# Performance work log

Measured on AMD Instinct MI355X. Metric: run time of the kernel, lower is better.

Reference implementation:

```python
import jax, jax.numpy as jnp
import numpy as np
from jax import lax

INPUT_SIZE = 32
HIDDEN = 64
BATCH = 8192
SEQ = 128


def _lstm_layer(x, w_ih, w_hh, b_ih, b_hh):
    """Single unidirectional LSTM layer, PyTorch gate order (i, f, g, o).
    x: [B, T, D] -> (outputs [B, T, H], final h [B, H])"""
    B = x.shape[0]
    H = w_hh.shape[1]
    # Precompute input contributions for all timesteps: [B, T, 4H]
    xg = jnp.einsum('btd,gd->btg', x, w_ih) + b_ih + b_hh

    def step(carry, xg_t):
        h, c = carry
        gates = xg_t + h @ w_hh.T  # [B, 4H]
        i, f, g, o = jnp.split(gates, 4, axis=-1)
        i = jax.nn.sigmoid(i)
        f = jax.nn.sigmoid(f)
        g = jnp.tanh(g)
        o = jax.nn.sigmoid(o)
        c = f * c + i * g
        h = o * jnp.tanh(c)
        return (h, c), h

    h0 = jnp.zeros((B, H), dtype=x.dtype)
    c0 = jnp.zeros((B, H), dtype=x.dtype)
    (h_n, _), hs = lax.scan(step, (h0, c0), jnp.swapaxes(xg, 0, 1))
    return jnp.swapaxes(hs, 0, 1), h_n


def setup_inputs() -> dict:
    key = jax.random.key(0)
    ks = jax.random.split(key, 12)
    H4 = 4 * HIDDEN
    s_ih0 = 1.0 / np.sqrt(INPUT_SIZE)
    s_h = 1.0 / np.sqrt(HIDDEN)
    x = jax.random.normal(ks[0], (BATCH, SEQ, INPUT_SIZE), dtype=jnp.float32)
    # Biases: zeros with forget-gate bias = 1 (per _init_weights)
    b = jnp.zeros((H4,), dtype=jnp.float32).at[HIDDEN:2 * HIDDEN].set(1.0)
    return {
        'x': x,
        'w_ih0': jax.random.uniform(ks[1], (H4, INPUT_SIZE), jnp.float32, -s_ih0, s_ih0),
        'w_hh0': jax.random.uniform(ks[2], (H4, HIDDEN), jnp.float32, -s_h, s_h),
        'b_ih0': b,
        'b_hh0': jnp.zeros((H4,), dtype=jnp.float32),
        'w_ih1': jax.random.uniform(ks[3], (H4, HIDDEN), jnp.float32, -s_h, s_h),
        'w_hh1': jax.random.uniform(ks[4], (H4, HIDDEN), jnp.float32, -s_h, s_h),
        'b_ih1': b,
        'b_hh1': jnp.zeros((H4,), dtype=jnp.float32),
        'fc_w': jax.random.uniform(ks[5], (1, HIDDEN), jnp.float32, -s_h, s_h),
        'fc_b': jnp.zeros((1,), dtype=jnp.float32),
    }


def reference(x, w_ih0, w_hh0, b_ih0, b_hh0, w_ih1, w_hh1, b_ih1, b_hh1, fc_w, fc_b):
    # 2-layer LSTM (inter-layer dropout is identity at inference)
    h1_seq, _ = _lstm_layer(x, w_ih0, w_hh0, b_ih0, b_hh0)
    _, h_final = _lstm_layer(h1_seq, w_ih1, w_hh1, b_ih1, b_hh1)
    # dropout(h_final) is identity in eval mode; final linear head -> squeeze
    logit = h_final @ fc_w.T + fc_b  # [B, 1]
    return logit.squeeze(-1)  # [B]
```

## Files before the change

### kernel.cpp

```cpp
#include <hip/hip_runtime.h>


#define TT  128
#define DIN 32
#define BT  16
#define L2E 1.44269504088896340736f

typedef _Float16 h8 __attribute__((ext_vector_type(8)));
typedef __fp16   p2 __attribute__((ext_vector_type(2)));
typedef float    f4 __attribute__((ext_vector_type(4)));

__device__ __forceinline__ h8 cvt8s(const float* p, float s) {
    float4 a = *(const float4*)p;
    float4 b = *(const float4*)(p + 4);
    union { h8 v; p2 q[4]; } u;
    u.q[0] = __builtin_amdgcn_cvt_pkrtz(a.x * s, a.y * s);
    u.q[1] = __builtin_amdgcn_cvt_pkrtz(a.z * s, a.w * s);
    u.q[2] = __builtin_amdgcn_cvt_pkrtz(b.x * s, b.y * s);
    u.q[3] = __builtin_amdgcn_cvt_pkrtz(b.z * s, b.w * s);
    return u.v;
}

__device__ __forceinline__ h8 pack8(const float4& a, const float4& b) {
    union { h8 v; p2 q[4]; } u;
    u.q[0] = __builtin_amdgcn_cvt_pkrtz(a.x, a.y);
    u.q[1] = __builtin_amdgcn_cvt_pkrtz(a.z, a.w);
    u.q[2] = __builtin_amdgcn_cvt_pkrtz(b.x, b.y);
    u.q[3] = __builtin_amdgcn_cvt_pkrtz(b.z, b.w);
    return u.v;
}

__device__ __forceinline__ float elem(const f4& acc, float& c) {
    float Ei = __builtin_amdgcn_exp2f(-acc[0]);
    float Ef = __builtin_amdgcn_exp2f(-acc[1]);
    float Eg = __builtin_amdgcn_exp2f(-acc[2]);
    float Eo = __builtin_amdgcn_exp2f(-acc[3]);
    float a = 1.f + Ei, b = 1.f + Eg, d = 1.f + Ef;
    float P = a * b;
    float N = c * P + (1.f - Eg) * d;
    c = N * __builtin_amdgcn_rcpf(P * d);
    float Ec = __builtin_amdgcn_exp2f(-2.f * L2E * c);
    return (1.f - Ec) * __builtin_amdgcn_rcpf((1.f + Ec) * (1.f + Eo));
}

__global__ __launch_bounds__(512, 4)
void lstm2_fused(const float* __restrict__ x,
                 const float* __restrict__ wih0, const float* __restrict__ whh0,
                 const float* __restrict__ bih0, const float* __restrict__ bhh0,
                 const float* __restrict__ wih1, const float* __restrict__ whh1,
                 const float* __restrict__ bih1, const float* __restrict__ bhh1,
                 const float* __restrict__ fcw,  const float* __restrict__ fcb,
                 float* __restrict__ out)
{
    const int tid  = threadIdx.x;
    const int lane = tid & 63;
    const int wv   = tid >> 6;
    const int bl   = lane & 15;
    const int kg   = lane >> 4;

    __shared__ alignas(16) unsigned short hb[2][2][BT * 64];
    __shared__ float wpart[8][BT];

    for (int i = tid; i < (int)(sizeof(hb) / 4); i += 512) ((int*)hb)[i] = 0;

    h8 W0[2][3], W1[2][4];
    f4 b0v[2], b1v[2];
    #pragma unroll
    for (int t = 0; t < 2; ++t) {
        const int hbse = 8 * wv + 4 * t;
        const int gam  = bl & 3;
        const int g    = 64 * gam + hbse + (bl >> 2);
        const float sc = (gam == 2) ? 2.f * L2E : L2E;
        W0[t][0] = cvt8s(wih0 + g * 32 + 8 * kg, sc);
        W0[t][1] = cvt8s(whh0 + g * 64 + 8 * kg, sc);
        W0[t][2] = cvt8s(whh0 + g * 64 + 32 + 8 * kg, sc);
        W1[t][0] = cvt8s(wih1 + g * 64 + 8 * kg, sc);
        W1[t][1] = cvt8s(wih1 + g * 64 + 32 + 8 * kg, sc);
        W1[t][2] = cvt8s(whh1 + g * 64 + 8 * kg, sc);
        W1[t][3] = cvt8s(whh1 + g * 64 + 32 + 8 * kg, sc);
        #pragma unroll
        for (int r = 0; r < 4; ++r) {
            const int gr = 64 * r + hbse + kg;
            const float scr = (r == 2) ? 2.f * L2E : L2E;
            b0v[t][r] = (bih0[gr] + bhh0[gr]) * scr;
            b1v[t][r] = (bih1[gr] + bhh1[gr]) * scr;
        }
    }

    const int bbase = blockIdx.x * BT;
    const float* xp = x + (size_t)(bbase + bl) * (TT * DIN) + 8 * kg;

    float c0[2] = {0.f, 0.f}, c1[2] = {0.f, 0.f}, h1f[2] = {0.f, 0.f};

    __syncthreads();

    const int swz = (bl & 7) << 4;
    char* lb = (char*)hb;
    const int rowoff = bl * 128;
    const int rd0 = rowoff + ((16 * kg) ^ swz);
    const int rd1 = rowoff + ((64 + 16 * kg) ^ swz);
    const int wro0 = rowoff + ((16 * wv + 2 * kg) ^ swz);
    const int wro1 = rowoff + ((16 * wv + 8 + 2 * kg) ^ swz);

    auto L0 = [&](const h8& xc, const h8& hr0, const h8& hr1, int wp) {
        #pragma unroll
        for (int t = 0; t < 2; ++t) {
            f4 acc = b0v[t];
            acc = __builtin_amdgcn_mfma_f32_16x16x32_f16(W0[t][1], hr0, acc, 0, 0, 0);
            acc = __builtin_amdgcn_mfma_f32_16x16x32_f16(W0[t][2], hr1, acc, 0, 0, 0);
            acc = __builtin_amdgcn_mfma_f32_16x16x32_f16(W0[t][0], xc,  acc, 0, 0, 0);
            float h = elem(acc, c0[t]);
            *(_Float16*)(lb + wp * 2048 + (t ? wro1 : wro0)) = (_Float16)h;
        }
    };

    auto L1 = [&](const h8& g0a, const h8& g0b, const h8& g1a, const h8& g1b,
                  int wp, bool store) {
        #pragma unroll
        for (int t = 0; t < 2; ++t) {
            f4 acc = b1v[t];
            acc = __builtin_amdgcn_mfma_f32_16x16x32_f16(W1[t][0], g0a, acc, 0, 0, 0);
            acc = __builtin_amdgcn_mfma_f32_16x16x32_f16(W1[t][1], g0b, acc, 0, 0, 0);
            acc = __builtin_amdgcn_mfma_f32_16x16x32_f16(W1[t][2], g1a, acc, 0, 0, 0);
            acc = __builtin_amdgcn_mfma_f32_16x16x32_f16(W1[t][3], g1b, acc, 0, 0, 0);
            float h = elem(acc, c1[t]);
            h1f[t] = h;
            if (store) *(_Float16*)(lb + 4096 + wp * 2048 + (t ? wro1 : wro0)) = (_Float16)h;
        }
    };

    h8 xcur;
    {
        float4 x0a = *(const float4*)(xp);
        float4 x0b = *(const float4*)(xp + 4);
        float4 xnA = *(const float4*)(xp + DIN);
        float4 xnB = *(const float4*)(xp + DIN + 4);
        h8 xc  = pack8(x0a, x0b);
        h8 hr0 = *(const h8*)(lb + 2048 + rd0);
        h8 hr1 = *(const h8*)(lb + 2048 + rd1);
        L0(xc, hr0, hr1, 0);
        xcur = pack8(xnA, xnB);
        __syncthreads();
    }

    for (int it = 1; it < TT; ++it) {
        const int wp = it & 1, rp = wp ^ 1;
        const int tn = (it + 1 < TT) ? it + 1 : TT - 1;
        float4 xnA = *(const float4*)(xp + tn * DIN);
        float4 xnB = *(const float4*)(xp + tn * DIN + 4);

        h8 hr0 = *(const h8*)(lb + rp * 2048 + rd0);
        h8 hr1 = *(const h8*)(lb + rp * 2048 + rd1);
        h8 g1a = *(const h8*)(lb + 4096 + rp * 2048 + rd0);
        h8 g1b = *(const h8*)(lb + 4096 + rp * 2048 + rd1);

        L0(xcur, hr0, hr1, wp);
        L1(hr0, hr1, g1a, g1b, wp, true);

        xcur = pack8(xnA, xnB);
        __syncthreads();
    }

    {
        const int rp = 1;
        h8 hr0 = *(const h8*)(lb + rp * 2048 + rd0);
        h8 hr1 = *(const h8*)(lb + rp * 2048 + rd1);
        h8 g1a = *(const h8*)(lb + 4096 + rp * 2048 + rd0);
        h8 g1b = *(const h8*)(lb + 4096 + rp * 2048 + rd1);
        L1(hr0, hr1, g1a, g1b, 0, false);
    }

    float part = h1f[0] * fcw[8 * wv + kg] + h1f[1] * fcw[8 * wv + 4 + kg];
    part += __shfl_xor(part, 16, 64);
    part += __shfl_xor(part, 32, 64);
    if (lane < 16) wpart[wv][lane] = part;
    __syncthreads();
    if (tid < BT) {
        float s = fcb[0];
        #pragma unroll
        for (int w = 0; w < 8; ++w) s += wpart[w][tid];
        out[bbase + tid] = s;
    }
}

extern "C" void kernel_launch(void* const* d_in, const int* in_sizes, int n_in,
                              void* d_out, int out_size, void* d_ws, size_t ws_size,
                              hipStream_t stream) {
    (void)in_sizes; (void)n_in; (void)d_ws; (void)ws_size; (void)out_size;
    lstm2_fused<<<dim3(8192 / BT), dim3(512), 0, stream>>>(
        (const float*)d_in[0],
        (const float*)d_in[1], (const float*)d_in[2],
        (const float*)d_in[3], (const float*)d_in[4],
        (const float*)d_in[5], (const float*)d_in[6],
        (const float*)d_in[7], (const float*)d_in[8],
        (const float*)d_in[9], (const float*)d_in[10],
        (float*)d_out);
}
```

Before: 184.9 us.

## Split LSTM layers into producer/consumer warp groups with LDS flag sync

Assigns waves 0-3 to layer 0 and waves 4-7 to layer 1, each computing four hidden tiles, so the two layers run as a pipeline instead of in lockstep. Per-step __syncthreads is replaced by LDS counters polled with s_sleep, and layer-0 outputs go into a 4-deep ring buffer so the producer can run ahead. The aim is to overlap the two layers' dependency chains and cut block-wide barrier cost. In exchange it adds spin-wait polling, more registers per wave (weights for four tiles), and relies on volatile LDS ordering being correct.

```diff
diff --git a/kernel.cpp b/kernel.cpp
--- a/kernel.cpp
+++ b/kernel.cpp
@@ -9,6 +9,8 @@
 typedef _Float16 h8 __attribute__((ext_vector_type(8)));
 typedef __fp16   p2 __attribute__((ext_vector_type(2)));
 typedef float    f4 __attribute__((ext_vector_type(4)));
+
+#define MFMA(A, B, C) __builtin_amdgcn_mfma_f32_16x16x32_f16((A), (B), (C), 0, 0, 0)
 
 __device__ __forceinline__ h8 cvt8s(const float* p, float s) {
     float4 a = *(const float4*)p;
@@ -41,6 +43,17 @@
     c = N * __builtin_amdgcn_rcpf(P * d);
     float Ec = __builtin_amdgcn_exp2f(-2.f * L2E * c);
     return (1.f - Ec) * __builtin_amdgcn_rcpf((1.f + Ec) * (1.f + Eo));
+}
+
+__device__ __forceinline__ void waitmin4(const volatile int* c, int target) {
+    for (;;) {
+        int m0 = c[0], m1 = c[1], m2 = c[2], m3 = c[3];
+        int m = min(min(m0, m1), min(m2, m3));
+        if (m >= target) break;
+        __builtin_amdgcn_s_sleep(1);
+    }
+    __builtin_amdgcn_sched_barrier(0);
+    asm volatile("" ::: "memory");
 }
 
 __global__ __launch_bounds__(512, 4)
@@ -58,129 +71,157 @@
     const int bl   = lane & 15;
     const int kg   = lane >> 4;
 
-    __shared__ alignas(16) unsigned short hb[2][2][BT * 64];
-    __shared__ float wpart[8][BT];
+    __shared__ alignas(16) unsigned short hb[6][BT * 64];
+    __shared__ alignas(16) int ctrP[4];
+    __shared__ alignas(16) int ctrC[4];
+    __shared__ float wpart[4][BT];
 
     for (int i = tid; i < (int)(sizeof(hb) / 4); i += 512) ((int*)hb)[i] = 0;
-
-    h8 W0[2][3], W1[2][4];
-    f4 b0v[2], b1v[2];
-    #pragma unroll
-    for (int t = 0; t < 2; ++t) {
-        const int hbse = 8 * wv + 4 * t;
-        const int gam  = bl & 3;
-        const int g    = 64 * gam + hbse + (bl >> 2);
-        const float sc = (gam == 2) ? 2.f * L2E : L2E;
-        W0[t][0] = cvt8s(wih0 + g * 32 + 8 * kg, sc);
-        W0[t][1] = cvt8s(whh0 + g * 64 + 8 * kg, sc);
-        W0[t][2] = cvt8s(whh0 + g * 64 + 32 + 8 * kg, sc);
-        W1[t][0] = cvt8s(wih1 + g * 64 + 8 * kg, sc);
-        W1[t][1] = cvt8s(wih1 + g * 64 + 32 + 8 * kg, sc);
-        W1[t][2] = cvt8s(whh1 + g * 64 + 8 * kg, sc);
-        W1[t][3] = cvt8s(whh1 + g * 64 + 32 + 8 * kg, sc);
-        #pragma unroll
-        for (int r = 0; r < 4; ++r) {
-            const int gr = 64 * r + hbse + kg;
-            const float scr = (r == 2) ? 2.f * L2E : L2E;
-            b0v[t][r] = (bih0[gr] + bhh0[gr]) * scr;
-            b1v[t][r] = (bih1[gr] + bhh1[gr]) * scr;
-        }
-    }
+    if (tid < 4) { ctrP[tid] = 0; ctrC[tid] = 0; }
 
     const int bbase = blockIdx.x * BT;
-    const float* xp = x + (size_t)(bbase + bl) * (TT * DIN) + 8 * kg;
-
-    float c0[2] = {0.f, 0.f}, c1[2] = {0.f, 0.f}, h1f[2] = {0.f, 0.f};
-
-    __syncthreads();
-
     const int swz = (bl & 7) << 4;
     char* lb = (char*)hb;
     const int rowoff = bl * 128;
     const int rd0 = rowoff + ((16 * kg) ^ swz);
     const int rd1 = rowoff + ((64 + 16 * kg) ^ swz);
-    const int wro0 = rowoff + ((16 * wv + 2 * kg) ^ swz);
-    const int wro1 = rowoff + ((16 * wv + 8 + 2 * kg) ^ swz);
-
-    auto L0 = [&](const h8& xc, const h8& hr0, const h8& hr1, int wp) {
+
+    volatile int* vP = ctrP;
+    volatile int* vC = ctrC;
+
+    __syncthreads();
+
+    if (wv < 4) {
+        const int w = wv;
+        h8 W0[4][3]; f4 b0v[4]; int wro[4];
         #pragma unroll
-        for (int t = 0; t < 2; ++t) {
-            f4 acc = b0v[t];
-            acc = __builtin_amdgcn_mfma_f32_16x16x32_f16(W0[t][1], hr0, acc, 0, 0, 0);
-            acc = __builtin_amdgcn_mfma_f32_16x16x32_f16(W0[t][2], hr1, acc, 0, 0, 0);
-            acc = __builtin_amdgcn_mfma_f32_16x16x32_f16(W0[t][0], xc,  acc, 0, 0, 0);
-            float h = elem(acc, c0[t]);
-            *(_Float16*)(lb + wp * 2048 + (t ? wro1 : wro0)) = (_Float16)h;
-        }
-    };
-
-    auto L1 = [&](const h8& g0a, const h8& g0b, const h8& g1a, const h8& g1b,
-                  int wp, bool store) {
+        for (int t = 0; t < 4; ++t) {
+            const int hbse = 16 * w + 4 * t;
+            const int gam  = bl & 3;
+            const int g    = 64 * gam + hbse + (bl >> 2);
+            const float sc = (gam == 2) ? 2.f * L2E : L2E;
+            W0[t][0] = cvt8s(wih0 + g * 32 + 8 * kg, sc);
+            W0[t][1] = cvt8s(whh0 + g * 64 + 8 * kg, sc);
+            W0[t][2] = cvt8s(whh0 + g * 64 + 32 + 8 * kg, sc);
+            #pragma unroll
+            for (int r = 0; r < 4; ++r) {
+                const int gr = 64 * r + hbse + kg;
+                const float scr = (r == 2) ? 2.f * L2E : L2E;
+                b0v[t][r] = (bih0[gr] + bhh0[gr]) * scr;
+            }
+            wro[t] = rowoff + ((32 * w + 8 * t + 2 * kg) ^ swz);
+        }
+
+        const float* xp = x + (size_t)(bbase + bl) * (TT * DIN) + 8 * kg;
+        h8 xcur = pack8(*(const float4*)xp, *(const float4*)(xp + 4));
+        float c0[4] = {0.f, 0.f, 0.f, 0.f};
+
+        for (int t = 0; t < TT; ++t) {
+            if (t)      waitmin4(vP, t);
+            if (t >= 4) waitmin4(vC, t - 3);
+
+            const char* src = lb + (((t - 1) & 3) * 2048);
+            h8 hr0 = *(const h8*)(src + rd0);
+            h8 hr1 = *(const h8*)(src + rd1);
+            const int tn = (t + 1 < TT) ? t + 1 : t;
+            float4 xnA = *(const float4*)(xp + tn * DIN);
+            float4 xnB = *(const float4*)(xp + tn * DIN + 4);
+
+            __builtin_amdgcn_s_setprio(1);
+            f4 acc[4];
+            #pragma unroll
+            for (int k = 0; k < 4; ++k) {
+                acc[k] = b0v[k];
+                acc[k] = MFMA(W0[k][1], hr0, acc[k]);
+                acc[k] = MFMA(W0[k][2], hr1, acc[k]);
+                acc[k] = MFMA(W0[k][0], xcur, acc[k]);
+            }
+            __builtin_amdgcn_s_setprio(0);
+
+            char* dst = lb + ((t & 3) * 2048);
+            #pragma unroll
+            for (int k = 0; k < 4; ++k) {
+                float h = elem(acc[k], c0[k]);
+                *(_Float16*)(dst + wro[k]) = (_Float16)h;
+            }
+
+            asm volatile("s_waitcnt lgkmcnt(0)" ::: "memory");
+            if (lane == 0) vP[w] = t + 1;
+            xcur = pack8(xnA, xnB);
+        }
+    } else {
+        const int w = wv - 4;
+        h8 W1[4][4]; f4 b1v[4]; int wro[4];
         #pragma unroll
-        for (int t = 0; t < 2; ++t) {
-            f4 acc = b1v[t];
-            acc = __builtin_amdgcn_mfma_f32_16x16x32_f16(W1[t][0], g0a, acc, 0, 0, 0);
-            acc = __builtin_amdgcn_mfma_f32_16x16x32_f16(W1[t][1], g0b, acc, 0, 0, 0);
-            acc = __builtin_amdgcn_mfma_f32_16x16x32_f16(W1[t][2], g1a, acc, 0, 0, 0);
-            acc = __builtin_amdgcn_mfma_f32_16x16x32_f16(W1[t][3], g1b, acc, 0, 0, 0);
-            float h = elem(acc, c1[t]);
-            h1f[t] = h;
-            if (store) *(_Float16*)(lb + 4096 + wp * 2048 + (t ? wro1 : wro0)) = (_Float16)h;
-        }
-    };
-
-    h8 xcur;
-    {
-        float4 x0a = *(const float4*)(xp);
-        float4 x0b = *(const float4*)(xp + 4);
-        float4 xnA = *(const float4*)(xp + DIN);
-        float4 xnB = *(const float4*)(xp + DIN + 4);
-        h8 xc  = pack8(x0a, x0b);
-        h8 hr0 = *(const h8*)(lb + 2048 + rd0);
-        h8 hr1 = *(const h8*)(lb + 2048 + rd1);
-        L0(xc, hr0, hr1, 0);
-        xcur = pack8(xnA, xnB);
-        __syncthreads();
+        for (int t = 0; t < 4; ++t) {
+            const int hbse = 16 * w + 4 * t;
+            const int gam  = bl & 3;
+            const int g    = 64 * gam + hbse + (bl >> 2);
+            const float sc = (gam == 2) ? 2.f * L2E : L2E;
+            W1[t][0] = cvt8s(wih1 + g * 64 + 8 * kg, sc);
+            W1[t][1] = cvt8s(wih1 + g * 64 + 32 + 8 * kg, sc);
+            W1[t][2] = cvt8s(whh1 + g * 64 + 8 * kg, sc);
+            W1[t][3] = cvt8s(whh1 + g * 64 + 32 + 8 * kg, sc);
+            #pragma unroll
+            for (int r = 0; r < 4; ++r) {
+                const int gr = 64 * r + hbse + kg;
+                const float scr = (r == 2) ? 2.f * L2E : L2E;
+                b1v[t][r] = (bih1[gr] + bhh1[gr]) * scr;
+            }
+            wro[t] = rowoff + ((32 * w + 8 * t + 2 * kg) ^ swz);
+        }
+
+        float c1[4] = {0.f, 0.f, 0.f, 0.f};
+        float h1f[4] = {0.f, 0.f, 0.f, 0.f};
+
+        for (int t = 0; t < TT; ++t) {
+            waitmin4(vP, t + 1);
+            if (t) waitmin4(vC, t);
+
+            const char* s0 = lb + ((t & 3) * 2048);
+            const char* s1 = lb + 8192 + (((t - 1) & 1) * 2048);
+            h8 g0a = *(const h8*)(s0 + rd0);
+            h8 g0b = *(const h8*)(s0 + rd1);
+            h8 g1a = *(const h8*)(s1 + rd0);
+            h8 g1b = *(const h8*)(s1 + rd1);
+
+            __builtin_amdgcn_s_setprio(1);
+            f4 acc[4];
+            #pragma unroll
+            for (int k = 0; k < 4; ++k) {
+                acc[k] = b1v[k];
+                acc[k] = MFMA(W1[k][0], g0a, acc[k]);
+                acc[k] = MFMA(W1[k][1], g0b, acc[k]);
+                acc[k] = MFMA(W1[k][2], g1a, acc[k]);
+                acc[k] = MFMA(W1[k][3], g1b, acc[k]);
+            }
+            __builtin_amdgcn_s_setprio(0);
+
+            char* dst = lb + 8192 + ((t & 1) * 2048);
+            #pragma unroll
+            for (int k = 0; k < 4; ++k) {
+                float h = elem(acc[k], c1[k]);
+                h1f[k] = h;
+                if (t < TT - 1) *(_Float16*)(dst + wro[k]) = (_Float16)h;
+            }
+
+            if (t < TT - 1) {
+                asm volatile("s_waitcnt lgkmcnt(0)" ::: "memory");
+                if (lane == 0) vC[w] = t + 1;
+            }
+        }
+
+        float part = 0.f;
+        #pragma unroll
+        for (int k = 0; k < 4; ++k) part += h1f[k] * fcw[16 * w + 4 * k + kg];
+        part += __shfl_xor(part, 16, 64);
+        part += __shfl_xor(part, 32, 64);
+        if (lane < 16) wpart[w][lane] = part;
     }
 
-    for (int it = 1; it < TT; ++it) {
-        const int wp = it & 1, rp = wp ^ 1;
-        const int tn = (it + 1 < TT) ? it + 1 : TT - 1;
-        float4 xnA = *(const float4*)(xp + tn * DIN);
-        float4 xnB = *(const float4*)(xp + tn * DIN + 4);
-
-        h8 hr0 = *(const h8*)(lb + rp * 2048 + rd0);
-        h8 hr1 = *(const h8*)(lb + rp * 2048 + rd1);
-        h8 g1a = *(const h8*)(lb + 4096 + rp * 2048 + rd0);
-        h8 g1b = *(const h8*)(lb + 4096 + rp * 2048 + rd1);
-
-        L0(xcur, hr0, hr1, wp);
-        L1(hr0, hr1, g1a, g1b, wp, true);
-
-        xcur = pack8(xnA, xnB);
-        __syncthreads();
-    }
-
-    {
-        const int rp = 1;
-        h8 hr0 = *(const h8*)(lb + rp * 2048 + rd0);
-        h8 hr1 = *(const h8*)(lb + rp * 2048 + rd1);
-        h8 g1a = *(const h8*)(lb + 4096 + rp * 2048 + rd0);
-        h8 g1b = *(const h8*)(lb + 4096 + rp * 2048 + rd1);
-        L1(hr0, hr1, g1a, g1b, 0, false);
-    }
-
-    float part = h1f[0] * fcw[8 * wv + kg] + h1f[1] * fcw[8 * wv + 4 + kg];
-    part += __shfl_xor(part, 16, 64);
-    part += __shfl_xor(part, 32, 64);
-    if (lane < 16) wpart[wv][lane] = part;
     __syncthreads();
-    if (tid < BT) {
-        float s = fcb[0];
-        #pragma unroll
-        for (int w = 0; w < 8; ++w) s += wpart[w][tid];
-        out[bbase + tid] = s;
-    }
+    if (tid < BT)
+        out[bbase + tid] = wpart[0][tid] + wpart[1][tid] + wpart[2][tid] + wpart[3][tid] + fcb[0];
 }
 
 extern "C" void kernel_launch(void* const* d_in, const int* in_sizes, int n_in,
```

Measured after the change: 280.7 us. 51.8% more time.

## Halve waves per block, give each wave four gate tiles with interleaved MFMA chains

Applied to the files above, without the earlier changes.

Cuts the block from 512 to 256 threads (4 waves), so each wave owns 16 hidden units (four 16x16 gate tiles) instead of 8, doubling the weight registers per thread. The step body issues all layer-0 and layer-1 MFMA chains before any elementwise work, so the independent accumulators can hide MFMA latency. The time loop is unrolled by two with constant buffer indices. This reduces per-barrier wave count and gives more ILP per wave, at the cost of higher register pressure and fewer resident waves (launch bounds 256,2).

```diff
diff --git a/kernel.cpp b/kernel.cpp
--- a/kernel.cpp
+++ b/kernel.cpp
@@ -9,6 +9,8 @@
 typedef _Float16 h8 __attribute__((ext_vector_type(8)));
 typedef __fp16   p2 __attribute__((ext_vector_type(2)));
 typedef float    f4 __attribute__((ext_vector_type(4)));
+
+#define MFMA(A, B, C) __builtin_amdgcn_mfma_f32_16x16x32_f16((A), (B), (C), 0, 0, 0)
 
 __device__ __forceinline__ h8 cvt8s(const float* p, float s) {
     float4 a = *(const float4*)p;
@@ -43,7 +45,7 @@
     return (1.f - Ec) * __builtin_amdgcn_rcpf((1.f + Ec) * (1.f + Eo));
 }
 
-__global__ __launch_bounds__(512, 4)
+__global__ __launch_bounds__(256, 2)
 void lstm2_fused(const float* __restrict__ x,
                  const float* __restrict__ wih0, const float* __restrict__ whh0,
                  const float* __restrict__ bih0, const float* __restrict__ bhh0,
@@ -59,15 +61,18 @@
     const int kg   = lane >> 4;
 
     __shared__ alignas(16) unsigned short hb[2][2][BT * 64];
-    __shared__ float wpart[8][BT];
-
-    for (int i = tid; i < (int)(sizeof(hb) / 4); i += 512) ((int*)hb)[i] = 0;
-
-    h8 W0[2][3], W1[2][4];
-    f4 b0v[2], b1v[2];
+    __shared__ float wpart[4][BT];
+
+    for (int i = tid; i < (int)(sizeof(hb) / 4); i += 256) ((int*)hb)[i] = 0;
+
+    h8 W0[4][3], W1[4][4];
+    f4 b0v[4], b1v[4];
+    int wro[4];
+    const int swz = (bl & 7) << 4;
+    const int rowoff = bl * 128;
     #pragma unroll
-    for (int t = 0; t < 2; ++t) {
-        const int hbse = 8 * wv + 4 * t;
+    for (int t = 0; t < 4; ++t) {
+        const int hbse = 16 * wv + 4 * t;
         const int gam  = bl & 3;
         const int g    = 64 * gam + hbse + (bl >> 2);
         const float sc = (gam == 2) ? 2.f * L2E : L2E;
@@ -85,51 +90,66 @@
             b0v[t][r] = (bih0[gr] + bhh0[gr]) * scr;
             b1v[t][r] = (bih1[gr] + bhh1[gr]) * scr;
         }
+        wro[t] = rowoff + ((32 * wv + 8 * t + 2 * kg) ^ swz);
     }
 
     const int bbase = blockIdx.x * BT;
     const float* xp = x + (size_t)(bbase + bl) * (TT * DIN) + 8 * kg;
 
-    float c0[2] = {0.f, 0.f}, c1[2] = {0.f, 0.f}, h1f[2] = {0.f, 0.f};
+    float c0[4] = {0.f, 0.f, 0.f, 0.f};
+    float c1[4] = {0.f, 0.f, 0.f, 0.f};
+    float h1f[4] = {0.f, 0.f, 0.f, 0.f};
 
     __syncthreads();
 
-    const int swz = (bl & 7) << 4;
     char* lb = (char*)hb;
-    const int rowoff = bl * 128;
     const int rd0 = rowoff + ((16 * kg) ^ swz);
     const int rd1 = rowoff + ((64 + 16 * kg) ^ swz);
-    const int wro0 = rowoff + ((16 * wv + 2 * kg) ^ swz);
-    const int wro1 = rowoff + ((16 * wv + 8 + 2 * kg) ^ swz);
-
-    auto L0 = [&](const h8& xc, const h8& hr0, const h8& hr1, int wp) {
-        #pragma unroll
-        for (int t = 0; t < 2; ++t) {
-            f4 acc = b0v[t];
-            acc = __builtin_amdgcn_mfma_f32_16x16x32_f16(W0[t][1], hr0, acc, 0, 0, 0);
-            acc = __builtin_amdgcn_mfma_f32_16x16x32_f16(W0[t][2], hr1, acc, 0, 0, 0);
-            acc = __builtin_amdgcn_mfma_f32_16x16x32_f16(W0[t][0], xc,  acc, 0, 0, 0);
-            float h = elem(acc, c0[t]);
-            *(_Float16*)(lb + wp * 2048 + (t ? wro1 : wro0)) = (_Float16)h;
-        }
+
+    h8 xcur;
+
+    auto STEP = [&](int wp, int rp, const float* xnext) {
+        float4 xnA, xnB;
+        if (xnext) { xnA = *(const float4*)xnext; xnB = *(const float4*)(xnext + 4); }
+
+        h8 hr0 = *(const h8*)(lb + rp * 2048 + rd0);
+        h8 hr1 = *(const h8*)(lb + rp * 2048 + rd1);
+        h8 g1a = *(const h8*)(lb + 4096 + rp * 2048 + rd0);
+        h8 g1b = *(const h8*)(lb + 4096 + rp * 2048 + rd1);
+
+        f4 a0[4], a1[4];
+        #pragma unroll
+        for (int k = 0; k < 4; ++k) {
+            a0[k] = b0v[k];
+            a0[k] = MFMA(W0[k][1], hr0, a0[k]);
+            a0[k] = MFMA(W0[k][2], hr1, a0[k]);
+            a0[k] = MFMA(W0[k][0], xcur, a0[k]);
+        }
+        #pragma unroll
+        for (int k = 0; k < 4; ++k) {
+            a1[k] = b1v[k];
+            a1[k] = MFMA(W1[k][0], hr0, a1[k]);
+            a1[k] = MFMA(W1[k][1], hr1, a1[k]);
+            a1[k] = MFMA(W1[k][2], g1a, a1[k]);
+            a1[k] = MFMA(W1[k][3], g1b, a1[k]);
+        }
+
+        #pragma unroll
+        for (int k = 0; k < 4; ++k) {
+            float h = elem(a0[k], c0[k]);
+            *(_Float16*)(lb + wp * 2048 + wro[k]) = (_Float16)h;
+        }
+        #pragma unroll
+        for (int k = 0; k < 4; ++k) {
+            float h = elem(a1[k], c1[k]);
+            h1f[k] = h;
+            *(_Float16*)(lb + 4096 + wp * 2048 + wro[k]) = (_Float16)h;
+        }
+
+        if (xnext) xcur = pack8(xnA, xnB);
+        __syncthreads();
     };
 
-    auto L1 = [&](const h8& g0a, const h8& g0b, const h8& g1a, const h8& g1b,
-                  int wp, bool store) {
-        #pragma unroll
-        for (int t = 0; t < 2; ++t) {
-            f4 acc = b1v[t];
-            acc = __builtin_amdgcn_mfma_f32_16x16x32_f16(W1[t][0], g0a, acc, 0, 0, 0);
-            acc = __builtin_amdgcn_mfma_f32_16x16x32_f16(W1[t][1], g0b, acc, 0, 0, 0);
-            acc = __builtin_amdgcn_mfma_f32_16x16x32_f16(W1[t][2], g1a, acc, 0, 0, 0);
-            acc = __builtin_amdgcn_mfma_f32_16x16x32_f16(W1[t][3], g1b, acc, 0, 0, 0);
-            float h = elem(acc, c1[t]);
-            h1f[t] = h;
-            if (store) *(_Float16*)(lb + 4096 + wp * 2048 + (t ? wro1 : wro0)) = (_Float16)h;
-        }
-    };
-
-    h8 xcur;
     {
         float4 x0a = *(const float4*)(xp);
         float4 x0b = *(const float4*)(xp + 4);
@@ -138,56 +158,61 @@
         h8 xc  = pack8(x0a, x0b);
         h8 hr0 = *(const h8*)(lb + 2048 + rd0);
         h8 hr1 = *(const h8*)(lb + 2048 + rd1);
-        L0(xc, hr0, hr1, 0);
+        f4 a0[4];
+        #pragma unroll
+        for (int k = 0; k < 4; ++k) {
+            a0[k] = b0v[k];
+            a0[k] = MFMA(W0[k][1], hr0, a0[k]);
+            a0[k] = MFMA(W0[k][2], hr1, a0[k]);
+            a0[k] = MFMA(W0[k][0], xc, a0[k]);
+        }
+        #pragma unroll
+        for (int k = 0; k < 4; ++k) {
+            float h = elem(a0[k], c0[k]);
+            *(_Float16*)(lb + 0 * 2048 + wro[k]) = (_Float16)h;
+        }
         xcur = pack8(xnA, xnB);
         __syncthreads();
     }
 
-    for (int it = 1; it < TT; ++it) {
-        const int wp = it & 1, rp = wp ^ 1;
-        const int tn = (it + 1 < TT) ? it + 1 : TT - 1;
-        float4 xnA = *(const float4*)(xp + tn * DIN);
-        float4 xnB = *(const float4*)(xp + tn * DIN + 4);
-
-        h8 hr0 = *(const h8*)(lb + rp * 2048 + rd0);
-        h8 hr1 = *(const h8*)(lb + rp * 2048 + rd1);
-        h8 g1a = *(const h8*)(lb + 4096 + rp * 2048 + rd0);
-        h8 g1b = *(const h8*)(lb + 4096 + rp * 2048 + rd1);
-
-        L0(xcur, hr0, hr1, wp);
-        L1(hr0, hr1, g1a, g1b, wp, true);
-
-        xcur = pack8(xnA, xnB);
-        __syncthreads();
-    }
+    for (int itp = 1; itp < TT - 1; itp += 2) {
+        STEP(1, 0, xp + (itp + 1) * DIN);
+        STEP(0, 1, xp + (itp + 2) * DIN);
+    }
+    STEP(1, 0, nullptr);
 
     {
-        const int rp = 1;
-        h8 hr0 = *(const h8*)(lb + rp * 2048 + rd0);
-        h8 hr1 = *(const h8*)(lb + rp * 2048 + rd1);
-        h8 g1a = *(const h8*)(lb + 4096 + rp * 2048 + rd0);
-        h8 g1b = *(const h8*)(lb + 4096 + rp * 2048 + rd1);
-        L1(hr0, hr1, g1a, g1b, 0, false);
-    }
-
-    float part = h1f[0] * fcw[8 * wv + kg] + h1f[1] * fcw[8 * wv + 4 + kg];
+        h8 hr0 = *(const h8*)(lb + 2048 + rd0);
+        h8 hr1 = *(const h8*)(lb + 2048 + rd1);
+        h8 g1a = *(const h8*)(lb + 4096 + 2048 + rd0);
+        h8 g1b = *(const h8*)(lb + 4096 + 2048 + rd1);
+        #pragma unroll
+        for (int k = 0; k < 4; ++k) {
+            f4 a1 = b1v[k];
+            a1 = MFMA(W1[k][0], hr0, a1);
+            a1 = MFMA(W1[k][1], hr1, a1);
+            a1 = MFMA(W1[k][2], g1a, a1);
+            a1 = MFMA(W1[k][3], g1b, a1);
+            h1f[k] = elem(a1, c1[k]);
+        }
+    }
+
+    float part = 0.f;
+    #pragma unroll
+    for (int k = 0; k < 4; ++k) part += h1f[k] * fcw[16 * wv + 4 * k + kg];
     part += __shfl_xor(part, 16, 64);
     part += __shfl_xor(part, 32, 64);
     if (lane < 16) wpart[wv][lane] = part;
     __syncthreads();
-    if (tid < BT) {
-        float s = fcb[0];
-        #pragma unroll
-        for (int w = 0; w < 8; ++w) s += wpart[w][tid];
-        out[bbase + tid] = s;
-    }
+    if (tid < BT)
+        out[bbase + tid] = wpart[0][tid] + wpart[1][tid] + wpart[2][tid] + wpart[3][tid] + fcb[0];
 }
 
 extern "C" void kernel_launch(void* const* d_in, const int* in_sizes, int n_in,
                               void* d_out, int out_size, void* d_ws, size_t ws_size,
                               hipStream_t stream) {
     (void)in_sizes; (void)n_in; (void)d_ws; (void)ws_size; (void)out_size;
-    lstm2_fused<<<dim3(8192 / BT), dim3(512), 0, stream>>>(
+    lstm2_fused<<<dim3(8192 / BT), dim3(256), 0, stream>>>(
         (const float*)d_in[0],
         (const float*)d_in[1], (const float*)d_in[2],
         (const float*)d_in[3], (const float*)d_in[4],
```

Measured after the change: 185.5 us. No clear change (+0.3%).
